# Optimization experiments

Measured on AMD Instinct MI355X. Metric: run time of the kernel, lower is better.

The kernel has to match this reference:

```python
import jax, jax.numpy as jnp
import numpy as np
from jax import lax

# Edit-distance-style DP alignment between a predicted sprite sequence xs and a
# target character sequence ys. Substitution cost for matching sprite s to char a
# is (1 - softmax(P, axis=1))[s, a]; the cost matrix is padded with an Inf row/col
# so padding tokens (index S / A) can never be matched. Gap moves (insert/delete,
# the (1,1)-step 'do nothing' costs) cost 1. Effective lengths are lengths-1.
#
# Recurrence: D[i,j] = min(D[i-1,j] + 1, D[i,j-1] + 1, D[i-1,j-1] + c[i,j]).
# Rows are computed with one lax.scan over i; the intra-row dependency
# D[i,j] = min(E[i,j], D[i,j-1]+1) is resolved with a cumulative min:
# D[i,j] = min_{k<=j}(E[i,k] - k) + j.


def _matching_loss(P, xs, ys, xl, yl):
    C = jnp.pad(1.0 - jax.nn.softmax(P, axis=1), ((0, 1), (0, 1)),
                constant_values=jnp.inf)                  # (S+1, A+1)
    cost = C[xs[:, :, None], ys[:, None, :]]              # (B, Lx, Ly)
    B, Lx, Ly = cost.shape
    j = jnp.arange(Ly + 1, dtype=cost.dtype)
    D0 = jnp.broadcast_to(j, (B, Ly + 1))                 # D[0, :] = j (all inserts)

    def step(Dprev, c_i):                                 # c_i: (B, Ly)
        # candidates that only depend on the previous row
        E = jnp.minimum(Dprev[:, 1:] + 1.0, Dprev[:, :-1] + c_i)   # (B, Ly)
        E_full = jnp.concatenate([Dprev[:, :1] + 1.0, E], axis=1)  # (B, Ly+1)
        # resolve left-neighbor dependency via min-plus prefix scan
        D = lax.cummin(E_full - j, axis=1) + j
        return D, D

    _, Drows = lax.scan(step, D0, jnp.swapaxes(cost, 0, 1))  # (Lx, B, Ly+1)
    Dall = jnp.concatenate([D0[None], Drows], axis=0)        # (Lx+1, B, Ly+1)
    return Dall[xl, jnp.arange(B), yl]                       # (B,) per-pair loss


def setup_inputs() -> dict:
    key = jax.random.key(0)
    kP, kx, ky, kxl, kyl = jax.random.split(key, 5)
    S, A = 128, 96
    B, Lx, Ly = 256, 512, 256
    P = jax.nn.softmax(jax.random.uniform(kP, (S, A), dtype=jnp.float32), axis=1)
    xs = jax.random.randint(kx, (B, Lx), 0, S, dtype=jnp.int32).astype(jnp.int64)
    ys = jax.random.randint(ky, (B, Ly), 0, A, dtype=jnp.int32).astype(jnp.int64)
    x_lengths = jax.random.randint(kxl, (B,), 2, Lx + 1, dtype=jnp.int32)
    y_lengths = jax.random.randint(kyl, (B,), 2, Ly + 1, dtype=jnp.int32)
    return {"P": P, "xs": xs, "ys": ys,
            "x_lengths": x_lengths, "y_lengths": y_lengths}


def reference(P, xs, ys, x_lengths, y_lengths):
    # forward passes (lengths - 1) into the matching loss
    return _matching_loss(P, xs, ys, x_lengths - 1, y_lengths - 1)
```

## Files before the change

kernel.cpp:

```cpp
#include <hip/hip_runtime.h>

#define S_DIM 128
#define A_DIM 96
#define B_DIM 256
#define LX 512
#define LY 256
#define PADL 64
#define PADR 96

template <int CTRL>
__device__ __forceinline__ float dpp_mov(float oldv, float src) {
    return __int_as_float(__builtin_amdgcn_update_dpp(
        __float_as_int(oldv), __float_as_int(src), CTRL, 0xF, 0xF, false));
}

__global__ __launch_bounds__(64) void softmax_kernel(const float* __restrict__ P,
                                                     float* __restrict__ C) {
    int row = blockIdx.x, lane = threadIdx.x;
    const float* p = P + row * A_DIM;
    float v0 = p[lane];
    float v1 = (lane < A_DIM - 64) ? p[64 + lane] : -1e30f;
    float m = fmaxf(v0, v1);
    #pragma unroll
    for (int d = 32; d > 0; d >>= 1) m = fmaxf(m, __shfl_xor(m, d));
    float e0 = expf(v0 - m);
    float e1 = (lane < A_DIM - 64) ? expf(v1 - m) : 0.0f;
    float s = e0 + e1;
    #pragma unroll
    for (int d = 32; d > 0; d >>= 1) s += __shfl_xor(s, d);
    float inv = 1.0f / s;
    C[row * A_DIM + lane] = -1.0f - e0 * inv;
    if (lane < A_DIM - 64) C[row * A_DIM + 64 + lane] = -1.0f - e1 * inv;
}

#define PHASE(Q0, Q1, Q2, Q3)                            \
    {                                                    \
        float Lf = dpp_mov<0x138>(0.0f, g3);             \
        float v0 = fminf(fminf(Lf, g0), pB0);            \
        float v1 = fminf(fminf(v0, g1), pB1);            \
        float v2 = fminf(fminf(v1, g2), pB2);            \
        float v3 = fminf(fminf(v2, g3), pB3);            \
        bool act = (unsigned)iu < xl_u;                  \
        g0 = act ? v0 : g0;                              \
        g1 = act ? v1 : g1;                              \
        g2 = act ? v2 : g2;                              \
        g3 = act ? v3 : g3;                              \
        iu += 1;                                         \
        pB0 = Lf + (Q0);                                 \
        pB1 = g0 + (Q1);                                 \
        pB2 = g1 + (Q2);                                 \
        pB3 = g2 + (Q3);                                 \
    }

#define SB() __builtin_amdgcn_sched_barrier(0x7)

__global__ __launch_bounds__(64) void dp_kernel(const float* __restrict__ C,
                                                const int* __restrict__ xs,
                                                const int* __restrict__ ys,
                                                const int* __restrict__ xlen,
                                                const int* __restrict__ ylen,
                                                float* __restrict__ out) {
    __shared__ float sC[S_DIM * A_DIM];
    __shared__ int sXbuf[PADL + LX + PADR];

    int b = blockIdx.x, lane = threadIdx.x;
    {
        const float4* Cg4 = (const float4*)C;
        float4* sC4 = (float4*)sC;
        #pragma unroll
        for (int k = 0; k < (S_DIM * A_DIM) / (4 * 64); ++k)
            sC4[lane + 64 * k] = Cg4[lane + 64 * k];
        const int* xsb = xs + b * LX;
        int* sXw = sXbuf + PADL;
        #pragma unroll
        for (int k = 0; k < LX / 64; ++k)
            sXw[lane + 64 * k] = xsb[lane + 64 * k] * (A_DIM * 4);
        sXbuf[lane] = 0;
        sXbuf[PADL + LX + lane] = 0;
        if (lane < PADR - 64) sXbuf[PADL + LX + 64 + lane] = 0;
    }
    __syncthreads();

    int xl = xlen[b] - 1;
    int yl = ylen[b] - 1;
    unsigned xl_u = (unsigned)xl;
    int4 yv = *(const int4*)(ys + b * LY + lane * 4);
    int yb0 = yv.x * 4, yb1 = yv.y * 4, yb2 = yv.z * 4, yb3 = yv.w * 4;
    int lane_ans = (yl - 1) >> 2;
    int t_end = xl + lane_ans;
    int iu = -lane;
    const int* sXp = sXbuf + PADL;
    const char* sCB = (const char*)sC;

#define LDC(XB, YB) (*(const float*)(sCB + (unsigned)((XB) + (YB))))

    int xm  = sXp[iu];
    int xa0 = sXp[iu + 1], xa1 = sXp[iu + 2], xa2 = sXp[iu + 3];
    int xv0 = sXp[iu + 4], xv1 = sXp[iu + 5], xv2 = sXp[iu + 6];
    float pB0 = LDC(xm, yb0), pB1 = LDC(xm, yb1), pB2 = LDC(xm, yb2), pB3 = LDC(xm, yb3);
    float s00 = LDC(xa0, yb0), s01 = LDC(xa0, yb1), s02 = LDC(xa0, yb2), s03 = LDC(xa0, yb3);
    float s10 = LDC(xa1, yb0), s11 = LDC(xa1, yb1), s12 = LDC(xa1, yb2), s13 = LDC(xa1, yb3);
    float s20 = LDC(xa2, yb0), s21 = LDC(xa2, yb1), s22 = LDC(xa2, yb2), s23 = LDC(xa2, yb3);
    float s30, s31, s32, s33;
    int xv3;
    float g0 = 0.f, g1 = 0.f, g2 = 0.f, g3 = 0.f;

    int T = 1;
    for (; T + 3 <= t_end; T += 4) {
        PHASE(s00, s01, s02, s03);
        SB();
        s30 = LDC(xv0, yb0); s31 = LDC(xv0, yb1);
        s32 = LDC(xv0, yb2); s33 = LDC(xv0, yb3);
        xv3 = sXp[iu + 6];
        SB();
        PHASE(s10, s11, s12, s13);
        SB();
        s00 = LDC(xv1, yb0); s01 = LDC(xv1, yb1);
        s02 = LDC(xv1, yb2); s03 = LDC(xv1, yb3);
        xv0 = sXp[iu + 6];
        SB();
        PHASE(s20, s21, s22, s23);
        SB();
        s10 = LDC(xv2, yb0); s11 = LDC(xv2, yb1);
        s12 = LDC(xv2, yb2); s13 = LDC(xv2, yb3);
        xv1 = sXp[iu + 6];
        SB();
        PHASE(s30, s31, s32, s33);
        SB();
        s20 = LDC(xv3, yb0); s21 = LDC(xv3, yb1);
        s22 = LDC(xv3, yb2); s23 = LDC(xv3, yb3);
        xv2 = sXp[iu + 6];
        SB();
    }
    if (T <= t_end) { PHASE(s00, s01, s02, s03); ++T; }
    if (T <= t_end) { PHASE(s10, s11, s12, s13); ++T; }
    if (T <= t_end) { PHASE(s20, s21, s22, s23); }

    if (lane == lane_ans) {
        int slot = (yl - 1) & 3;
        float r = (slot == 0) ? g0 : (slot == 1) ? g1 : (slot == 2) ? g2 : g3;
        out[b] = r + (float)(xl + yl);
    }
}

extern "C" void kernel_launch(void* const* d_in, const int* in_sizes, int n_in,
                              void* d_out, int out_size, void* d_ws, size_t ws_size,
                              hipStream_t stream) {
    const float* P  = (const float*)d_in[0];
    const int* xs   = (const int*)d_in[1];
    const int* ys   = (const int*)d_in[2];
    const int* xlen = (const int*)d_in[3];
    const int* ylen = (const int*)d_in[4];
    float* out = (float*)d_out;
    float* C = (float*)d_ws;

    softmax_kernel<<<S_DIM, 64, 0, stream>>>(P, C);
    dp_kernel<<<B_DIM, 64, 0, stream>>>(C, xs, ys, xlen, ylen, out);
}
```

Measured before the change: 94.15 us.

## Shorten DP critical path with tree mins and Inf-padded sentinel rows

Restructures the per-phase min chain so most of the fminf work depends only on the previous values and cost loads, leaving just a short dependent chain after the cross-lane DPP move. The per-step active-mask selects are dropped: out-of-range rows now read an Inf cost row appended to the shared cost table, so masking is no longer needed. Loads for the next phase are issued before each PHASE, with a pointer increment replacing per-phase index arithmetic. This relies on the Inf sentinel reproducing the old masking semantics, including at the trailing zero padding.

Result: faster. 91.84 us (-2.5%).

```diff
diff --git a/kernel.cpp b/kernel.cpp
--- a/kernel.cpp
+++ b/kernel.cpp
@@ -33,23 +33,23 @@
     if (lane < A_DIM - 64) C[row * A_DIM + 64 + lane] = -1.0f - e1 * inv;
 }
 
-#define PHASE(Q0, Q1, Q2, Q3)                            \
-    {                                                    \
-        float Lf = dpp_mov<0x138>(0.0f, g3);             \
-        float v0 = fminf(fminf(Lf, g0), pB0);            \
-        float v1 = fminf(fminf(v0, g1), pB1);            \
-        float v2 = fminf(fminf(v1, g2), pB2);            \
-        float v3 = fminf(fminf(v2, g3), pB3);            \
-        bool act = (unsigned)iu < xl_u;                  \
-        g0 = act ? v0 : g0;                              \
-        g1 = act ? v1 : g1;                              \
-        g2 = act ? v2 : g2;                              \
-        g3 = act ? v3 : g3;                              \
-        iu += 1;                                         \
-        pB0 = Lf + (Q0);                                 \
-        pB1 = g0 + (Q1);                                 \
-        pB2 = g1 + (Q2);                                 \
-        pB3 = g2 + (Q3);                                 \
+#define PHASE(Q0, Q1, Q2, Q3)                               \
+    {                                                       \
+        float m1  = fminf(g1, pB1);                         \
+        float m2  = fminf(g2, pB2);                         \
+        float m3  = fminf(g3, pB3);                         \
+        float t01 = fminf(fminf(g0, pB0), m1);              \
+        float t23 = fminf(m2, m3);                          \
+        float Lf  = dpp_mov<0x138>(0.0f, g3);               \
+        float v0  = fminf(fminf(Lf, g0), pB0);              \
+        float v1  = fminf(Lf, t01);                         \
+        float v2  = fminf(v1, m2);                          \
+        float v3  = fminf(v1, t23);                         \
+        g0 = v0; g1 = v1; g2 = v2; g3 = v3;                 \
+        pB0 = Lf + (Q0);                                    \
+        pB1 = v0 + (Q1);                                    \
+        pB2 = v1 + (Q2);                                    \
+        pB3 = v2 + (Q3);                                    \
     }
 
 #define SB() __builtin_amdgcn_sched_barrier(0x7)
@@ -60,7 +60,7 @@
                                                 const int* __restrict__ xlen,
                                                 const int* __restrict__ ylen,
                                                 float* __restrict__ out) {
-    __shared__ float sC[S_DIM * A_DIM];
+    __shared__ float sC[(S_DIM + 1) * A_DIM];
     __shared__ int sXbuf[PADL + LX + PADR];
 
     int b = blockIdx.x, lane = threadIdx.x;
@@ -70,12 +70,15 @@
         #pragma unroll
         for (int k = 0; k < (S_DIM * A_DIM) / (4 * 64); ++k)
             sC4[lane + 64 * k] = Cg4[lane + 64 * k];
+        float INF = __builtin_inff();
+        sC[S_DIM * A_DIM + lane] = INF;
+        if (lane < A_DIM - 64) sC[S_DIM * A_DIM + 64 + lane] = INF;
         const int* xsb = xs + b * LX;
         int* sXw = sXbuf + PADL;
         #pragma unroll
         for (int k = 0; k < LX / 64; ++k)
             sXw[lane + 64 * k] = xsb[lane + 64 * k] * (A_DIM * 4);
-        sXbuf[lane] = 0;
+        sXbuf[lane] = S_DIM * A_DIM * 4;
         sXbuf[PADL + LX + lane] = 0;
         if (lane < PADR - 64) sXbuf[PADL + LX + 64 + lane] = 0;
     }
@@ -83,54 +86,53 @@
 
     int xl = xlen[b] - 1;
     int yl = ylen[b] - 1;
-    unsigned xl_u = (unsigned)xl;
     int4 yv = *(const int4*)(ys + b * LY + lane * 4);
     int yb0 = yv.x * 4, yb1 = yv.y * 4, yb2 = yv.z * 4, yb3 = yv.w * 4;
     int lane_ans = (yl - 1) >> 2;
     int t_end = xl + lane_ans;
-    int iu = -lane;
-    const int* sXp = sXbuf + PADL;
+    const int* sXp0 = sXbuf + PADL - lane;
     const char* sCB = (const char*)sC;
 
 #define LDC(XB, YB) (*(const float*)(sCB + (unsigned)((XB) + (YB))))
 
-    int xm  = sXp[iu];
-    int xa0 = sXp[iu + 1], xa1 = sXp[iu + 2], xa2 = sXp[iu + 3];
-    int xv0 = sXp[iu + 4], xv1 = sXp[iu + 5], xv2 = sXp[iu + 6];
+    int xm  = sXp0[0];
+    int xa0 = sXp0[1], xa1 = sXp0[2], xa2 = sXp0[3];
+    int xv0 = sXp0[4], xv1 = sXp0[5], xv2 = sXp0[6], xv3 = sXp0[7];
+    const int* sxp8 = sXp0 + 8;
     float pB0 = LDC(xm, yb0), pB1 = LDC(xm, yb1), pB2 = LDC(xm, yb2), pB3 = LDC(xm, yb3);
     float s00 = LDC(xa0, yb0), s01 = LDC(xa0, yb1), s02 = LDC(xa0, yb2), s03 = LDC(xa0, yb3);
     float s10 = LDC(xa1, yb0), s11 = LDC(xa1, yb1), s12 = LDC(xa1, yb2), s13 = LDC(xa1, yb3);
     float s20 = LDC(xa2, yb0), s21 = LDC(xa2, yb1), s22 = LDC(xa2, yb2), s23 = LDC(xa2, yb3);
     float s30, s31, s32, s33;
-    int xv3;
     float g0 = 0.f, g1 = 0.f, g2 = 0.f, g3 = 0.f;
 
     int T = 1;
     for (; T + 3 <= t_end; T += 4) {
+        s30 = LDC(xv0, yb0); s31 = LDC(xv0, yb1);
+        s32 = LDC(xv0, yb2); s33 = LDC(xv0, yb3);
+        xv0 = sxp8[0];
+        SB();
         PHASE(s00, s01, s02, s03);
         SB();
-        s30 = LDC(xv0, yb0); s31 = LDC(xv0, yb1);
-        s32 = LDC(xv0, yb2); s33 = LDC(xv0, yb3);
-        xv3 = sXp[iu + 6];
+        s00 = LDC(xv1, yb0); s01 = LDC(xv1, yb1);
+        s02 = LDC(xv1, yb2); s03 = LDC(xv1, yb3);
+        xv1 = sxp8[1];
         SB();
         PHASE(s10, s11, s12, s13);
         SB();
-        s00 = LDC(xv1, yb0); s01 = LDC(xv1, yb1);
-        s02 = LDC(xv1, yb2); s03 = LDC(xv1, yb3);
-        xv0 = sXp[iu + 6];
+        s10 = LDC(xv2, yb0); s11 = LDC(xv2, yb1);
+        s12 = LDC(xv2, yb2); s13 = LDC(xv2, yb3);
+        xv2 = sxp8[2];
         SB();
         PHASE(s20, s21, s22, s23);
         SB();
-        s10 = LDC(xv2, yb0); s11 = LDC(xv2, yb1);
-        s12 = LDC(xv2, yb2); s13 = LDC(xv2, yb3);
-        xv1 = sXp[iu + 6];
+        s20 = LDC(xv3, yb0); s21 = LDC(xv3, yb1);
+        s22 = LDC(xv3, yb2); s23 = LDC(xv3, yb3);
+        xv3 = sxp8[3];
         SB();
         PHASE(s30, s31, s32, s33);
         SB();
-        s20 = LDC(xv3, yb0); s21 = LDC(xv3, yb1);
-        s22 = LDC(xv3, yb2); s23 = LDC(xv3, yb3);
-        xv2 = sXp[iu + 6];
-        SB();
+        sxp8 += 4;
     }
     if (T <= t_end) { PHASE(s00, s01, s02, s03); ++T; }
     if (T <= t_end) { PHASE(s10, s11, s12, s13); ++T; }
```
